# Performance work log

Measured on AMD Instinct MI355X. Metric: run time of the kernel, lower is better.

The kernel has to match this reference:

```python
import jax, jax.numpy as jnp
import numpy as np

EMBED_DIM = 1024
NUM_HEADS = 16
HEAD_DIM = EMBED_DIM // NUM_HEADS
LN_EPS = 1e-5


def setup_inputs() -> dict:
    key = jax.random.key(0)
    ks = jax.random.split(key, 6)
    b, s, d = 2, 2048, EMBED_DIM
    scale = 1.0 / np.sqrt(d)
    x = jax.random.normal(ks[0], (b, s, d), dtype=jnp.float32)
    w_qkv = jax.random.normal(ks[1], (d, 3 * d), dtype=jnp.float32) * scale
    b_qkv = jax.random.normal(ks[2], (3 * d,), dtype=jnp.float32) * 0.02
    w_out = jax.random.normal(ks[3], (d, d), dtype=jnp.float32) * scale
    b_out = jax.random.normal(ks[4], (d,), dtype=jnp.float32) * 0.02
    gamma = jnp.ones((d,), dtype=jnp.float32)
    ln_beta = jnp.zeros((d,), dtype=jnp.float32)
    beta = jax.random.normal(ks[5], (), dtype=jnp.float32) * 0.1
    return {"x": x, "w_qkv": w_qkv, "b_qkv": b_qkv, "w_out": w_out,
            "b_out": b_out, "gamma": gamma, "ln_beta": ln_beta, "beta": beta}


def _layernorm(x, gamma, ln_beta):
    mu = jnp.mean(x, axis=-1, keepdims=True)
    var = jnp.mean(jnp.square(x - mu), axis=-1, keepdims=True)
    return (x - mu) * jax.lax.rsqrt(var + LN_EPS) * gamma + ln_beta


def reference(x, w_qkv, b_qkv, w_out, b_out, gamma, ln_beta, beta):
    b, s, d = x.shape
    h, hd = NUM_HEADS, HEAD_DIM
    residual = x
    xn = _layernorm(x, gamma, ln_beta)
    qkv = xn @ w_qkv + b_qkv                       # [b, s, 3d]
    qkv = qkv.reshape(b, s, 3, h, hd)
    q = jnp.transpose(qkv[:, :, 0], (0, 2, 1, 3))  # [b, h, s, hd]
    k = jnp.transpose(qkv[:, :, 1], (0, 2, 1, 3))
    v = jnp.transpose(qkv[:, :, 2], (0, 2, 1, 3))
    attn = jnp.einsum('bhqd,bhkd->bhqk', q, k) / np.sqrt(hd)
    idx = jnp.arange(s)
    dist = jnp.abs(idx[None, :] - idx[:, None]).astype(attn.dtype)  # [s, s]
    attn = attn + beta * jnp.log1p(dist)[None, None, :, :]
    probs = jax.nn.softmax(attn, axis=-1)
    ctx = jnp.einsum('bhqk,bhkd->bhqd', probs, v)  # [b, h, s, hd]
    ctx = jnp.transpose(ctx, (0, 2, 1, 3)).reshape(b, s, d)
    return residual + ctx @ w_out + b_out
```

## Files before the change

### kernel.cpp

```cpp
#include <hip/hip_runtime.h>

#define SEQ 2048
#define DIM 1024
#define NHEAD 16
#define HDIM 64
#define NTOK 4096
#define N3D 3072

typedef __attribute__((ext_vector_type(8))) short bf16x8;
typedef __attribute__((ext_vector_type(4))) float floatx4;
typedef __attribute__((ext_vector_type(4))) unsigned short ushortx4;

__device__ __forceinline__ unsigned short f2bf(float f) {
    unsigned int u = __builtin_bit_cast(unsigned int, f);
    u += 0x7FFFu + ((u >> 16) & 1u);
    return (unsigned short)(u >> 16);
}

__device__ __forceinline__ void async_copy16(const void* g, const void* l) {
    __builtin_amdgcn_global_load_lds(
        (const __attribute__((address_space(1))) unsigned int*)(unsigned long long)g,
        (__attribute__((address_space(3))) unsigned int*)(unsigned int)(unsigned long long)l,
        16, 0, 0);
}

#define MFMA_BF16(a, b, c) __builtin_amdgcn_mfma_f32_16x16x32_bf16((a), (b), (c), 0, 0, 0)

__global__ __launch_bounds__(256)
void transpose_cvt(const float* __restrict__ src, unsigned short* __restrict__ dst,
                   int rows, int cols) {
    __shared__ float tile[32][33];
    const int c0 = blockIdx.x * 32, r0 = blockIdx.y * 32;
    const int tx = threadIdx.x & 31, ty = threadIdx.x >> 5;
    for (int i = 0; i < 4; ++i) {
        int r = ty + i * 8;
        tile[r][tx] = src[(size_t)(r0 + r) * cols + c0 + tx];
    }
    __syncthreads();
    for (int i = 0; i < 4; ++i) {
        int rr = ty + i * 8;
        dst[(size_t)(c0 + rr) * rows + r0 + tx] = f2bf(tile[tx][rr]);
    }
}

__global__ __launch_bounds__(256)
void ln_kernel(const float* __restrict__ x, const float* __restrict__ gamma,
               const float* __restrict__ lnb, unsigned short* __restrict__ xn) {
    const int row = blockIdx.x;
    const int tid = threadIdx.x;
    const float* xr = x + (size_t)row * DIM;
    float4 v = ((const float4*)xr)[tid];
    float s = v.x + v.y + v.z + v.w;
    float s2 = v.x * v.x + v.y * v.y + v.z * v.z + v.w * v.w;
    for (int off = 1; off < 64; off <<= 1) {
        s += __shfl_xor(s, off, 64);
        s2 += __shfl_xor(s2, off, 64);
    }
    __shared__ float red[8];
    const int wave = tid >> 6, lane = tid & 63;
    if (lane == 0) { red[wave] = s; red[4 + wave] = s2; }
    __syncthreads();
    s = red[0] + red[1] + red[2] + red[3];
    s2 = red[4] + red[5] + red[6] + red[7];
    const float mu = s * (1.0f / DIM);
    const float var = s2 * (1.0f / DIM) - mu * mu;
    const float rstd = rsqrtf(var + 1e-5f);
    float4 g = ((const float4*)gamma)[tid];
    float4 bb = ((const float4*)lnb)[tid];
    unsigned short* o = xn + (size_t)row * DIM + tid * 4;
    o[0] = f2bf((v.x - mu) * rstd * g.x + bb.x);
    o[1] = f2bf((v.y - mu) * rstd * g.y + bb.y);
    o[2] = f2bf((v.z - mu) * rstd * g.z + bb.z);
    o[3] = f2bf((v.w - mu) * rstd * g.w + bb.w);
}

__global__ __launch_bounds__(256)
void qkv_gemm(const unsigned short* __restrict__ A, const unsigned short* __restrict__ Bt,
              const float* __restrict__ bias, unsigned short* __restrict__ qo,
              unsigned short* __restrict__ ko, unsigned short* __restrict__ vTo) {
    __shared__ unsigned short Asm[128 * 32];
    __shared__ unsigned short Bsm[128 * 32];
    const int tid = threadIdx.x;
    const int wave = tid >> 6, lane = tid & 63;
    const int quad = lane >> 4, r16 = lane & 15;
    const int m0 = blockIdx.y * 128, n0 = blockIdx.x * 128;
    const int wm = (wave & 1) * 64, wn = (wave >> 1) * 64;
    floatx4 acc[4][4] = {};
    for (int k0 = 0; k0 < DIM; k0 += 32) {
        __syncthreads();
        for (int p = 0; p < 2; ++p) {
            int s = tid + p * 256;
            int r = s >> 2, c8 = (s & 3) << 3;
            async_copy16(A + (size_t)(m0 + r) * DIM + k0 + c8, Asm + s * 8);
            async_copy16(Bt + (size_t)(n0 + r) * DIM + k0 + c8, Bsm + s * 8);
        }
        __syncthreads();
        bf16x8 af[4], bfr[4];
        for (int i = 0; i < 4; ++i)
            af[i] = *(const bf16x8*)(Asm + (wm + i * 16 + r16) * 32 + quad * 8);
        for (int j = 0; j < 4; ++j)
            bfr[j] = *(const bf16x8*)(Bsm + (wn + j * 16 + r16) * 32 + quad * 8);
        for (int i = 0; i < 4; ++i)
            for (int j = 0; j < 4; ++j)
                acc[i][j] = MFMA_BF16(af[i], bfr[j], acc[i][j]);
    }
    for (int j = 0; j < 4; ++j) {
        int n = n0 + wn + j * 16 + r16;
        float bn = bias[n];
        int part = n >> 10, nn = n & 1023;
        int head = nn >> 6, hdi = nn & 63;
        for (int i = 0; i < 4; ++i) {
            int mbase = m0 + wm + i * 16 + quad * 4;
            int bIdx = mbase >> 11, sIdx = mbase & 2047;
            if (part == 2) {
                ushortx4 pack;
                for (int e = 0; e < 4; ++e) pack[e] = f2bf(acc[i][j][e] + bn);
                *(ushortx4*)(vTo + ((size_t)(bIdx * NHEAD + head) * HDIM + hdi) * SEQ + sIdx) = pack;
            } else {
                unsigned short* dst = (part == 0) ? qo : ko;
                for (int e = 0; e < 4; ++e)
                    dst[((size_t)(bIdx * NHEAD + head) * SEQ + sIdx + e) * HDIM + hdi] =
                        f2bf(acc[i][j][e] + bn);
            }
        }
    }
}

__global__ __launch_bounds__(512)
void attn_kernel(const unsigned short* __restrict__ qg, const unsigned short* __restrict__ kg,
                 const unsigned short* __restrict__ vTg, const float* __restrict__ betap,
                 unsigned short* __restrict__ ctx) {
    __shared__ unsigned short QP[128][72];
    __shared__ unsigned short Kd[2][64 * 64];
    __shared__ unsigned short Vd[2][64 * 64];
    __shared__ float logt[SEQ];

    const int tid = threadIdx.x;
    const int wave = tid >> 6, lane = tid & 63;
    const int quad = lane >> 4, r16 = lane & 15;
    const int bh = blockIdx.y, qt = blockIdx.x;
    const int qBase = qt * 128;
    const float betaV = betap[0];
    const float L2E = 1.44269504f;
    const float c1 = 0.125f * L2E;

    for (int i = tid; i < SEQ; i += 512)
        logt[i] = betaV * log1pf((float)i) * L2E - 20.0f;

    const unsigned short* qptr = qg + ((size_t)bh * SEQ + qBase) * HDIM;
    for (int s = tid; s < 1024; s += 512) {
        int r = s >> 3, c8 = (s & 7) << 3;
        *(bf16x8*)(&QP[r][c8]) = *(const bf16x8*)(qptr + r * HDIM + c8);
    }

    const int sr = tid >> 3;
    const int scg = (tid & 7) ^ (sr & 7);
    const unsigned short* kbh = kg + (size_t)bh * SEQ * HDIM;
    const unsigned short* vbh = vTg + (size_t)bh * HDIM * SEQ;
    async_copy16(kbh + (size_t)sr * HDIM + scg * 8, &Kd[0][tid * 8]);
    async_copy16(vbh + (size_t)sr * SEQ + scg * 8, &Vd[0][tid * 8]);
    __syncthreads();

    bf16x8 qf0 = *(const bf16x8*)(&QP[wave * 16 + r16][quad * 8]);
    bf16x8 qf1 = *(const bf16x8*)(&QP[wave * 16 + r16][32 + quad * 8]);

    const bf16x8 onesv = {0x3F80, 0x3F80, 0x3F80, 0x3F80, 0x3F80, 0x3F80, 0x3F80, 0x3F80};

    floatx4 o[5] = {};
    const int qWaveBase = qBase + wave * 16;
    const int qrow0 = qWaveBase + quad * 4;

    for (int kt0 = 0; kt0 < SEQ; kt0 += 64) {
        const int buf = (kt0 >> 6) & 1;
        if (kt0 + 64 < SEQ) {
            async_copy16(kbh + (size_t)(kt0 + 64 + sr) * HDIM + scg * 8, &Kd[buf ^ 1][tid * 8]);
            async_copy16(vbh + (size_t)sr * SEQ + kt0 + 64 + scg * 8, &Vd[buf ^ 1][tid * 8]);
        }

        floatx4 sc[4];
        for (int ct = 0; ct < 4; ++ct) {
            int rK = ct * 16 + r16;
            const unsigned short* kb = &Kd[buf][rK * 64];
            bf16x8 kf0 = *(const bf16x8*)(kb + ((quad ^ (rK & 7)) << 3));
            bf16x8 kf1 = *(const bf16x8*)(kb + (((quad ^ 4) ^ (rK & 7)) << 3));
            floatx4 z = {0.f, 0.f, 0.f, 0.f};
            z = MFMA_BF16(qf0, kf0, z);
            z = MFMA_BF16(qf1, kf1, z);
            sc[ct] = z;
        }
        for (int ct = 0; ct < 4; ++ct) {
            const int keyTile = kt0 + ct * 16;
            const int key = keyTile + r16;
            if (qWaveBase >= keyTile + 16) {
                const float* lp = &logt[qrow0 - key];
                for (int i = 0; i < 4; ++i)
                    sc[ct][i] = __builtin_amdgcn_exp2f(sc[ct][i] * c1 + lp[i]);
            } else if (keyTile >= qWaveBase + 16) {
                const float* lp = &logt[key - qrow0 - 3];
                for (int i = 0; i < 4; ++i)
                    sc[ct][i] = __builtin_amdgcn_exp2f(sc[ct][i] * c1 + lp[3 - i]);
            } else {
                for (int i = 0; i < 4; ++i) {
                    int dist = qrow0 + i - key;
                    dist = dist < 0 ? -dist : dist;
                    sc[ct][i] = __builtin_amdgcn_exp2f(sc[ct][i] * c1 + logt[dist]);
                }
            }
        }
        for (int ct = 0; ct < 4; ++ct)
            for (int i = 0; i < 4; ++i)
                QP[wave * 16 + quad * 4 + i][ct * 16 + r16] = f2bf(sc[ct][i]);
        bf16x8 pf0 = *(const bf16x8*)(&QP[wave * 16 + r16][quad * 8]);
        bf16x8 pf1 = *(const bf16x8*)(&QP[wave * 16 + r16][32 + quad * 8]);
        for (int nt = 0; nt < 4; ++nt) {
            int rV = nt * 16 + r16;
            const unsigned short* vb = &Vd[buf][rV * 64];
            bf16x8 vf0 = *(const bf16x8*)(vb + ((quad ^ (rV & 7)) << 3));
            bf16x8 vf1 = *(const bf16x8*)(vb + (((quad ^ 4) ^ (rV & 7)) << 3));
            o[nt] = MFMA_BF16(pf0, vf0, o[nt]);
            o[nt] = MFMA_BF16(pf1, vf1, o[nt]);
        }
        o[4] = MFMA_BF16(pf0, onesv, o[4]);
        o[4] = MFMA_BF16(pf1, onesv, o[4]);

        __syncthreads();
    }

    const int b_ = bh >> 4, h_ = bh & 15;
    for (int i = 0; i < 4; ++i) {
        float inv = 1.0f / o[4][i];
        int qi = qBase + wave * 16 + quad * 4 + i;
        for (int nt = 0; nt < 4; ++nt) {
            int d = nt * 16 + r16;
            ctx[((size_t)(b_ * SEQ + qi)) * DIM + h_ * HDIM + d] = f2bf(o[nt][i] * inv);
        }
    }
}

__global__ __launch_bounds__(256)
void out_gemm(const unsigned short* __restrict__ A, const unsigned short* __restrict__ Bt,
              const float* __restrict__ bias, const float* __restrict__ resid,
              float* __restrict__ out) {
    __shared__ unsigned short Asm[128 * 32];
    __shared__ unsigned short Bsm[64 * 32];
    const int tid = threadIdx.x;
    const int wave = tid >> 6, lane = tid & 63;
    const int quad = lane >> 4, r16 = lane & 15;
    const int m0 = blockIdx.y * 128, n0 = blockIdx.x * 64;
    const int wm = (wave & 1) * 64, wn = (wave >> 1) * 32;
    floatx4 acc[4][2] = {};
    for (int k0 = 0; k0 < DIM; k0 += 32) {
        __syncthreads();
        for (int p = 0; p < 2; ++p) {
            int s = tid + p * 256;
            int r = s >> 2, c8 = (s & 3) << 3;
            async_copy16(A + (size_t)(m0 + r) * DIM + k0 + c8, Asm + s * 8);
        }
        {
            int r = tid >> 2, c8 = (tid & 3) << 3;
            async_copy16(Bt + (size_t)(n0 + r) * DIM + k0 + c8, Bsm + tid * 8);
        }
        __syncthreads();
        bf16x8 af[4], bfr[2];
        for (int i = 0; i < 4; ++i)
            af[i] = *(const bf16x8*)(Asm + (wm + i * 16 + r16) * 32 + quad * 8);
        for (int j = 0; j < 2; ++j)
            bfr[j] = *(const bf16x8*)(Bsm + (wn + j * 16 + r16) * 32 + quad * 8);
        for (int i = 0; i < 4; ++i)
            for (int j = 0; j < 2; ++j)
                acc[i][j] = MFMA_BF16(af[i], bfr[j], acc[i][j]);
    }
    for (int i = 0; i < 4; ++i)
        for (int j = 0; j < 2; ++j)
            for (int e = 0; e < 4; ++e) {
                int m = m0 + wm + i * 16 + quad * 4 + e;
                int n = n0 + wn + j * 16 + r16;
                out[(size_t)m * DIM + n] = acc[i][j][e] + bias[n] + resid[(size_t)m * DIM + n];
            }
}

extern "C" void kernel_launch(void* const* d_in, const int* in_sizes, int n_in,
                              void* d_out, int out_size, void* d_ws, size_t ws_size,
                              hipStream_t stream) {
    const float* x     = (const float*)d_in[0];
    const float* w_qkv = (const float*)d_in[1];
    const float* b_qkv = (const float*)d_in[2];
    const float* w_out = (const float*)d_in[3];
    const float* b_out = (const float*)d_in[4];
    const float* gamma = (const float*)d_in[5];
    const float* ln_b  = (const float*)d_in[6];
    const float* beta  = (const float*)d_in[7];
    float* out = (float*)d_out;

    char* ws = (char*)d_ws;
    const size_t MB = 1u << 20;
    unsigned short* xn    = (unsigned short*)(ws);
    unsigned short* wqkvT = (unsigned short*)(ws + 8 * MB);
    unsigned short* woutT = (unsigned short*)(ws + 14 * MB);
    unsigned short* qb    = (unsigned short*)(ws + 16 * MB);
    unsigned short* kb    = (unsigned short*)(ws + 24 * MB);
    unsigned short* vTb   = (unsigned short*)(ws + 32 * MB);
    unsigned short* ctx   = xn;

    transpose_cvt<<<dim3(96, 32), 256, 0, stream>>>(w_qkv, wqkvT, DIM, N3D);
    transpose_cvt<<<dim3(32, 32), 256, 0, stream>>>(w_out, woutT, DIM, DIM);
    ln_kernel<<<NTOK, 256, 0, stream>>>(x, gamma, ln_b, xn);
    qkv_gemm<<<dim3(24, 32), 256, 0, stream>>>(xn, wqkvT, b_qkv, qb, kb, vTb);
    attn_kernel<<<dim3(SEQ / 128, 32), 512, 0, stream>>>(qb, kb, vTb, beta, ctx);
    out_gemm<<<dim3(16, 32), 256, 0, stream>>>(ctx, woutT, b_out, x, out);
}
```

Measured before the change: 229.8 us.

## Split attention over key halves and build P in registers via bpermute

The attention grid gains a second dimension that splits the key range in half. Each block writes unnormalized bf16 partial outputs plus row sums, and a new combine kernel adds the halves and normalizes them before the output GEMM. The QK MFMA operands are swapped so scores come out transposed, which lets the probability fragment be assembled with ds_bpermute and packed bf16 conversion instead of a round trip through the QP shared tile. That tile is removed, and launch bounds request higher occupancy. The aim is more parallelism and less LDS traffic, at the cost of an extra kernel launch and extra global traffic for the partial outputs.

```diff
diff --git a/kernel.cpp b/kernel.cpp
--- a/kernel.cpp
+++ b/kernel.cpp
@@ -10,11 +10,22 @@
 typedef __attribute__((ext_vector_type(8))) short bf16x8;
 typedef __attribute__((ext_vector_type(4))) float floatx4;
 typedef __attribute__((ext_vector_type(4))) unsigned short ushortx4;
+typedef __attribute__((ext_vector_type(4))) int intx4;
 
 __device__ __forceinline__ unsigned short f2bf(float f) {
     unsigned int u = __builtin_bit_cast(unsigned int, f);
     u += 0x7FFFu + ((u >> 16) & 1u);
     return (unsigned short)(u >> 16);
+}
+
+__device__ __forceinline__ unsigned int pack_bf16(float a, float b) {
+#if __has_builtin(__builtin_amdgcn_cvt_pk_bf16_f32)
+    typedef __attribute__((ext_vector_type(2))) __bf16 bf16x2t;
+    bf16x2t t = __builtin_amdgcn_cvt_pk_bf16_f32(a, b);
+    return __builtin_bit_cast(unsigned int, t);
+#else
+    return (unsigned int)f2bf(a) | ((unsigned int)f2bf(b) << 16);
+#endif
 }
 
 __device__ __forceinline__ void async_copy16(const void* g, const void* l) {
@@ -126,11 +137,10 @@
     }
 }
 
-__global__ __launch_bounds__(512)
+__global__ __launch_bounds__(512, 8)
 void attn_kernel(const unsigned short* __restrict__ qg, const unsigned short* __restrict__ kg,
                  const unsigned short* __restrict__ vTg, const float* __restrict__ betap,
-                 unsigned short* __restrict__ ctx) {
-    __shared__ unsigned short QP[128][72];
+                 unsigned short* __restrict__ opart, float* __restrict__ lpart) {
     __shared__ unsigned short Kd[2][64 * 64];
     __shared__ unsigned short Vd[2][64 * 64];
     __shared__ float logt[SEQ];
@@ -138,8 +148,9 @@
     const int tid = threadIdx.x;
     const int wave = tid >> 6, lane = tid & 63;
     const int quad = lane >> 4, r16 = lane & 15;
-    const int bh = blockIdx.y, qt = blockIdx.x;
+    const int bh = blockIdx.y, qt = blockIdx.x, ks = blockIdx.z;
     const int qBase = qt * 128;
+    const int kBase = ks * (SEQ / 2);
     const float betaV = betap[0];
     const float L2E = 1.44269504f;
     const float c1 = 0.125f * L2E;
@@ -147,32 +158,32 @@
     for (int i = tid; i < SEQ; i += 512)
         logt[i] = betaV * log1pf((float)i) * L2E - 20.0f;
 
-    const unsigned short* qptr = qg + ((size_t)bh * SEQ + qBase) * HDIM;
-    for (int s = tid; s < 1024; s += 512) {
-        int r = s >> 3, c8 = (s & 7) << 3;
-        *(bf16x8*)(&QP[r][c8]) = *(const bf16x8*)(qptr + r * HDIM + c8);
-    }
+    const unsigned short* qrow_p = qg + ((size_t)bh * SEQ + qBase + wave * 16 + r16) * HDIM;
+    bf16x8 qf0 = *(const bf16x8*)(qrow_p + quad * 8);
+    bf16x8 qf1 = *(const bf16x8*)(qrow_p + 32 + quad * 8);
 
     const int sr = tid >> 3;
     const int scg = (tid & 7) ^ (sr & 7);
     const unsigned short* kbh = kg + (size_t)bh * SEQ * HDIM;
     const unsigned short* vbh = vTg + (size_t)bh * HDIM * SEQ;
-    async_copy16(kbh + (size_t)sr * HDIM + scg * 8, &Kd[0][tid * 8]);
-    async_copy16(vbh + (size_t)sr * SEQ + scg * 8, &Vd[0][tid * 8]);
+    async_copy16(kbh + (size_t)(kBase + sr) * HDIM + scg * 8, &Kd[0][tid * 8]);
+    async_copy16(vbh + (size_t)sr * SEQ + kBase + scg * 8, &Vd[0][tid * 8]);
     __syncthreads();
 
-    bf16x8 qf0 = *(const bf16x8*)(&QP[wave * 16 + r16][quad * 8]);
-    bf16x8 qf1 = *(const bf16x8*)(&QP[wave * 16 + r16][32 + quad * 8]);
-
     const bf16x8 onesv = {0x3F80, 0x3F80, 0x3F80, 0x3F80, 0x3F80, 0x3F80, 0x3F80, 0x3F80};
-
-    floatx4 o[5] = {};
+    const int idx_lo = ((quad & 1) * 32 + r16) * 4;
+    const int idx_hi = ((quad & 1) * 32 + 16 + r16) * 4;
+    const bool hi_ct = quad >= 2;
+
+    floatx4 o[4] = {};
+    floatx4 o4 = {};
+    const int qrow = qBase + wave * 16 + r16;
     const int qWaveBase = qBase + wave * 16;
-    const int qrow0 = qWaveBase + quad * 4;
-
-    for (int kt0 = 0; kt0 < SEQ; kt0 += 64) {
-        const int buf = (kt0 >> 6) & 1;
-        if (kt0 + 64 < SEQ) {
+
+    for (int kt = 0; kt < SEQ / 2; kt += 64) {
+        const int kt0 = kBase + kt;
+        const int buf = (kt >> 6) & 1;
+        if (kt + 64 < SEQ / 2) {
             async_copy16(kbh + (size_t)(kt0 + 64 + sr) * HDIM + scg * 8, &Kd[buf ^ 1][tid * 8]);
             async_copy16(vbh + (size_t)sr * SEQ + kt0 + 64 + scg * 8, &Vd[buf ^ 1][tid * 8]);
         }
@@ -184,57 +195,89 @@
             bf16x8 kf0 = *(const bf16x8*)(kb + ((quad ^ (rK & 7)) << 3));
             bf16x8 kf1 = *(const bf16x8*)(kb + (((quad ^ 4) ^ (rK & 7)) << 3));
             floatx4 z = {0.f, 0.f, 0.f, 0.f};
-            z = MFMA_BF16(qf0, kf0, z);
-            z = MFMA_BF16(qf1, kf1, z);
+            z = MFMA_BF16(kf0, qf0, z);
+            z = MFMA_BF16(kf1, qf1, z);
             sc[ct] = z;
         }
         for (int ct = 0; ct < 4; ++ct) {
             const int keyTile = kt0 + ct * 16;
-            const int key = keyTile + r16;
+            const int key0 = keyTile + quad * 4;
             if (qWaveBase >= keyTile + 16) {
-                const float* lp = &logt[qrow0 - key];
+                const float* lp = &logt[qrow - key0 - 3];
+                for (int i = 0; i < 4; ++i)
+                    sc[ct][i] = __builtin_amdgcn_exp2f(sc[ct][i] * c1 + lp[3 - i]);
+            } else if (keyTile >= qWaveBase + 16) {
+                const float* lp = &logt[key0 - qrow];
                 for (int i = 0; i < 4; ++i)
                     sc[ct][i] = __builtin_amdgcn_exp2f(sc[ct][i] * c1 + lp[i]);
-            } else if (keyTile >= qWaveBase + 16) {
-                const float* lp = &logt[key - qrow0 - 3];
-                for (int i = 0; i < 4; ++i)
-                    sc[ct][i] = __builtin_amdgcn_exp2f(sc[ct][i] * c1 + lp[3 - i]);
             } else {
                 for (int i = 0; i < 4; ++i) {
-                    int dist = qrow0 + i - key;
-                    dist = dist < 0 ? -dist : dist;
-                    sc[ct][i] = __builtin_amdgcn_exp2f(sc[ct][i] * c1 + logt[dist]);
+                    int d = key0 + i - qrow;
+                    d = d < 0 ? -d : d;
+                    sc[ct][i] = __builtin_amdgcn_exp2f(sc[ct][i] * c1 + logt[d]);
                 }
             }
         }
-        for (int ct = 0; ct < 4; ++ct)
-            for (int i = 0; i < 4; ++i)
-                QP[wave * 16 + quad * 4 + i][ct * 16 + r16] = f2bf(sc[ct][i]);
-        bf16x8 pf0 = *(const bf16x8*)(&QP[wave * 16 + r16][quad * 8]);
-        bf16x8 pf1 = *(const bf16x8*)(&QP[wave * 16 + r16][32 + quad * 8]);
-        for (int nt = 0; nt < 4; ++nt) {
-            int rV = nt * 16 + r16;
-            const unsigned short* vb = &Vd[buf][rV * 64];
-            bf16x8 vf0 = *(const bf16x8*)(vb + ((quad ^ (rV & 7)) << 3));
-            bf16x8 vf1 = *(const bf16x8*)(vb + (((quad ^ 4) ^ (rV & 7)) << 3));
-            o[nt] = MFMA_BF16(pf0, vf0, o[nt]);
-            o[nt] = MFMA_BF16(pf1, vf1, o[nt]);
-        }
-        o[4] = MFMA_BF16(pf0, onesv, o[4]);
-        o[4] = MFMA_BF16(pf1, onesv, o[4]);
-
-        __syncthreads();
-    }
-
+        unsigned int pk[4][2];
+        for (int ct = 0; ct < 4; ++ct) {
+            pk[ct][0] = pack_bf16(sc[ct][0], sc[ct][1]);
+            pk[ct][1] = pack_bf16(sc[ct][2], sc[ct][3]);
+        }
+        for (int h = 0; h < 2; ++h) {
+            const int cA = 2 * h, cB = 2 * h + 1;
+            int b0a = __builtin_amdgcn_ds_bpermute(idx_lo, (int)pk[cA][0]);
+            int b0b = __builtin_amdgcn_ds_bpermute(idx_lo, (int)pk[cB][0]);
+            int b1a = __builtin_amdgcn_ds_bpermute(idx_lo, (int)pk[cA][1]);
+            int b1b = __builtin_amdgcn_ds_bpermute(idx_lo, (int)pk[cB][1]);
+            int b2a = __builtin_amdgcn_ds_bpermute(idx_hi, (int)pk[cA][0]);
+            int b2b = __builtin_amdgcn_ds_bpermute(idx_hi, (int)pk[cB][0]);
+            int b3a = __builtin_amdgcn_ds_bpermute(idx_hi, (int)pk[cA][1]);
+            int b3b = __builtin_amdgcn_ds_bpermute(idx_hi, (int)pk[cB][1]);
+            intx4 pb_i = {hi_ct ? b0b : b0a, hi_ct ? b1b : b1a,
+                          hi_ct ? b2b : b2a, hi_ct ? b3b : b3a};
+            bf16x8 pb = __builtin_bit_cast(bf16x8, pb_i);
+            for (int nt = 0; nt < 4; ++nt) {
+                int rV = nt * 16 + r16;
+                const unsigned short* vb = &Vd[buf][rV * 64];
+                bf16x8 vf = *(const bf16x8*)(vb + (((quad + 4 * h) ^ (rV & 7)) << 3));
+                o[nt] = MFMA_BF16(vf, pb, o[nt]);
+            }
+            o4 = MFMA_BF16(onesv, pb, o4);
+        }
+        __syncthreads();
+    }
+
+    unsigned short* op = opart + (size_t)ks * NTOK * DIM;
     const int b_ = bh >> 4, h_ = bh & 15;
+    const size_t rowoff = ((size_t)(b_ * SEQ + qrow)) * DIM + h_ * HDIM;
+    for (int nt = 0; nt < 4; ++nt) {
+        ushortx4 pck;
+        for (int i = 0; i < 4; ++i) pck[i] = f2bf(o[nt][i]);
+        *(ushortx4*)(op + rowoff + nt * 16 + quad * 4) = pck;
+    }
+    if (quad == 0)
+        lpart[(size_t)ks * NHEAD * 2 * SEQ + (size_t)bh * SEQ + qrow] = o4[0];
+}
+
+__global__ __launch_bounds__(256)
+void attn_combine(const unsigned short* __restrict__ oA, unsigned short* __restrict__ oB,
+                  const float* __restrict__ lA, const float* __restrict__ lB) {
+    const int row = blockIdx.x;
+    const int col = threadIdx.x * 4;
+    const int b_ = row >> 11, q = row & 2047;
+    const int head = col >> 6;
+    const int li = (b_ * NHEAD + head) * SEQ + q;
+    const float inv = 1.0f / (lA[li] + lB[li]);
+    const size_t off = (size_t)row * DIM + col;
+    ushortx4 a = *(const ushortx4*)(oA + off);
+    ushortx4 b = *(const ushortx4*)(oB + off);
+    ushortx4 r;
     for (int i = 0; i < 4; ++i) {
-        float inv = 1.0f / o[4][i];
-        int qi = qBase + wave * 16 + quad * 4 + i;
-        for (int nt = 0; nt < 4; ++nt) {
-            int d = nt * 16 + r16;
-            ctx[((size_t)(b_ * SEQ + qi)) * DIM + h_ * HDIM + d] = f2bf(o[nt][i] * inv);
-        }
-    }
+        float fa = __builtin_bit_cast(float, (unsigned int)(unsigned short)a[i] << 16);
+        float fb = __builtin_bit_cast(float, (unsigned int)(unsigned short)b[i] << 16);
+        r[i] = f2bf((fa + fb) * inv);
+    }
+    *(ushortx4*)(oB + off) = r;
 }
 
 __global__ __launch_bounds__(256)
@@ -295,17 +338,20 @@
     char* ws = (char*)d_ws;
     const size_t MB = 1u << 20;
     unsigned short* xn    = (unsigned short*)(ws);
-    unsigned short* wqkvT = (unsigned short*)(ws + 8 * MB);
-    unsigned short* woutT = (unsigned short*)(ws + 14 * MB);
-    unsigned short* qb    = (unsigned short*)(ws + 16 * MB);
-    unsigned short* kb    = (unsigned short*)(ws + 24 * MB);
-    unsigned short* vTb   = (unsigned short*)(ws + 32 * MB);
-    unsigned short* ctx   = xn;
+    unsigned short* oA    = (unsigned short*)(ws);
+    unsigned short* oB    = (unsigned short*)(ws + 8 * MB);
+    unsigned short* wqkvT = (unsigned short*)(ws + 16 * MB);
+    float*          lprt  = (float*)(ws + 16 * MB);
+    unsigned short* woutT = (unsigned short*)(ws + 22 * MB);
+    unsigned short* qb    = (unsigned short*)(ws + 24 * MB);
+    unsigned short* kb    = (unsigned short*)(ws + 32 * MB);
+    unsigned short* vTb   = (unsigned short*)(ws + 40 * MB);
 
     transpose_cvt<<<dim3(96, 32), 256, 0, stream>>>(w_qkv, wqkvT, DIM, N3D);
     transpose_cvt<<<dim3(32, 32), 256, 0, stream>>>(w_out, woutT, DIM, DIM);
     ln_kernel<<<NTOK, 256, 0, stream>>>(x, gamma, ln_b, xn);
     qkv_gemm<<<dim3(24, 32), 256, 0, stream>>>(xn, wqkvT, b_qkv, qb, kb, vTb);
-    attn_kernel<<<dim3(SEQ / 128, 32), 512, 0, stream>>>(qb, kb, vTb, beta, ctx);
-    out_gemm<<<dim3(16, 32), 256, 0, stream>>>(ctx, woutT, b_out, x, out);
-}
+    attn_kernel<<<dim3(SEQ / 128, 32, 2), 512, 0, stream>>>(qb, kb, vTb, beta, oA, lprt);
+    attn_combine<<<NTOK, 256, 0, stream>>>(oA, oB, lprt, lprt + 32 * SEQ);
+    out_gemm<<<dim3(16, 32), 256, 0, stream>>>(oB, woutT, b_out, x, out);
+}
```

New measurement: 249.8 us. +8.7%, slower.

## Compute transposed scores to keep P in registers and drop LDS round-trip

Applied to the files above, without the earlier changes.

The attention kernel now computes S^T (K as the A operand, Q as B), so each lane's softmax outputs line up with the B operand of a 16x16x16 MFMA for P·V. That removes the LDS write/read of P and the QP buffer. Each wave now handles 32 query rows with 256 threads per block, so K/V fragments loaded from LDS are reused across two query tiles. The log-bias table is stored as paired float2 entries so one read serves two lookups, and ctx stores are vectorized. The cost is more accumulator registers per wave and the use of the smaller-K MFMA variant.

```diff
diff --git a/kernel.cpp b/kernel.cpp
--- a/kernel.cpp
+++ b/kernel.cpp
@@ -8,13 +8,19 @@
 #define N3D 3072
 
 typedef __attribute__((ext_vector_type(8))) short bf16x8;
+typedef __attribute__((ext_vector_type(4))) short bf16x4;
 typedef __attribute__((ext_vector_type(4))) float floatx4;
 typedef __attribute__((ext_vector_type(4))) unsigned short ushortx4;
+typedef __attribute__((ext_vector_type(2))) int intx2;
 
 __device__ __forceinline__ unsigned short f2bf(float f) {
     unsigned int u = __builtin_bit_cast(unsigned int, f);
     u += 0x7FFFu + ((u >> 16) & 1u);
     return (unsigned short)(u >> 16);
+}
+
+__device__ __forceinline__ unsigned int pack_bf16(float a, float b) {
+    return (unsigned int)f2bf(a) | ((unsigned int)f2bf(b) << 16);
 }
 
 __device__ __forceinline__ void async_copy16(const void* g, const void* l) {
@@ -25,6 +31,7 @@
 }
 
 #define MFMA_BF16(a, b, c) __builtin_amdgcn_mfma_f32_16x16x32_bf16((a), (b), (c), 0, 0, 0)
+#define MFMA16(a, b, c) __builtin_amdgcn_mfma_f32_16x16x16bf16_1k((a), (b), (c), 0, 0, 0)
 
 __global__ __launch_bounds__(256)
 void transpose_cvt(const float* __restrict__ src, unsigned short* __restrict__ dst,
@@ -126,14 +133,13 @@
     }
 }
 
-__global__ __launch_bounds__(512)
+__global__ __launch_bounds__(256)
 void attn_kernel(const unsigned short* __restrict__ qg, const unsigned short* __restrict__ kg,
                  const unsigned short* __restrict__ vTg, const float* __restrict__ betap,
                  unsigned short* __restrict__ ctx) {
-    __shared__ unsigned short QP[128][72];
     __shared__ unsigned short Kd[2][64 * 64];
     __shared__ unsigned short Vd[2][64 * 64];
-    __shared__ float logt[SEQ];
+    __shared__ float2 L2t[SEQ];
 
     const int tid = threadIdx.x;
     const int wave = tid >> 6, lane = tid & 63;
@@ -144,13 +150,23 @@
     const float L2E = 1.44269504f;
     const float c1 = 0.125f * L2E;
 
-    for (int i = tid; i < SEQ; i += 512)
-        logt[i] = betaV * log1pf((float)i) * L2E - 20.0f;
-
-    const unsigned short* qptr = qg + ((size_t)bh * SEQ + qBase) * HDIM;
-    for (int s = tid; s < 1024; s += 512) {
-        int r = s >> 3, c8 = (s & 7) << 3;
-        *(bf16x8*)(&QP[r][c8]) = *(const bf16x8*)(qptr + r * HDIM + c8);
+    for (int t = tid; t < SEQ; t += 256) {
+        float fa = betaV * log1pf((float)t) * L2E - 20.0f;
+        int t1 = (t + 1 < SEQ) ? t + 1 : SEQ - 1;
+        float fb = betaV * log1pf((float)t1) * L2E - 20.0f;
+        L2t[t] = make_float2(fa, fb);
+    }
+    const float* Ff = (const float*)L2t;
+
+    bf16x8 qf[2][2];
+    {
+        const unsigned short* qp0 =
+            qg + ((size_t)bh * SEQ + qBase + wave * 32 + r16) * HDIM;
+        qf[0][0] = *(const bf16x8*)(qp0 + quad * 8);
+        qf[0][1] = *(const bf16x8*)(qp0 + 32 + quad * 8);
+        const unsigned short* qp1 = qp0 + 16 * HDIM;
+        qf[1][0] = *(const bf16x8*)(qp1 + quad * 8);
+        qf[1][1] = *(const bf16x8*)(qp1 + 32 + quad * 8);
     }
 
     const int sr = tid >> 3;
@@ -158,81 +174,99 @@
     const unsigned short* kbh = kg + (size_t)bh * SEQ * HDIM;
     const unsigned short* vbh = vTg + (size_t)bh * HDIM * SEQ;
     async_copy16(kbh + (size_t)sr * HDIM + scg * 8, &Kd[0][tid * 8]);
+    async_copy16(kbh + (size_t)(sr + 32) * HDIM + scg * 8, &Kd[0][2048 + tid * 8]);
     async_copy16(vbh + (size_t)sr * SEQ + scg * 8, &Vd[0][tid * 8]);
+    async_copy16(vbh + (size_t)(sr + 32) * SEQ + scg * 8, &Vd[0][2048 + tid * 8]);
     __syncthreads();
 
-    bf16x8 qf0 = *(const bf16x8*)(&QP[wave * 16 + r16][quad * 8]);
-    bf16x8 qf1 = *(const bf16x8*)(&QP[wave * 16 + r16][32 + quad * 8]);
-
-    const bf16x8 onesv = {0x3F80, 0x3F80, 0x3F80, 0x3F80, 0x3F80, 0x3F80, 0x3F80, 0x3F80};
-
-    floatx4 o[5] = {};
-    const int qWaveBase = qBase + wave * 16;
-    const int qrow0 = qWaveBase + quad * 4;
+    const bf16x4 ones4 = {0x3F80, 0x3F80, 0x3F80, 0x3F80};
+
+    floatx4 o[2][4] = {};
+    floatx4 o4[2] = {};
+    const int qWB0 = qBase + wave * 32;
+    const int qrow0 = qWB0 + r16;
 
     for (int kt0 = 0; kt0 < SEQ; kt0 += 64) {
         const int buf = (kt0 >> 6) & 1;
         if (kt0 + 64 < SEQ) {
-            async_copy16(kbh + (size_t)(kt0 + 64 + sr) * HDIM + scg * 8, &Kd[buf ^ 1][tid * 8]);
+            const unsigned short* kp = kbh + (size_t)(kt0 + 64) * HDIM;
+            async_copy16(kp + (size_t)sr * HDIM + scg * 8, &Kd[buf ^ 1][tid * 8]);
+            async_copy16(kp + (size_t)(sr + 32) * HDIM + scg * 8, &Kd[buf ^ 1][2048 + tid * 8]);
             async_copy16(vbh + (size_t)sr * SEQ + kt0 + 64 + scg * 8, &Vd[buf ^ 1][tid * 8]);
-        }
-
-        floatx4 sc[4];
+            async_copy16(vbh + (size_t)(sr + 32) * SEQ + kt0 + 64 + scg * 8,
+                         &Vd[buf ^ 1][2048 + tid * 8]);
+        }
+
+        floatx4 sc[2][4];
         for (int ct = 0; ct < 4; ++ct) {
             int rK = ct * 16 + r16;
             const unsigned short* kb = &Kd[buf][rK * 64];
             bf16x8 kf0 = *(const bf16x8*)(kb + ((quad ^ (rK & 7)) << 3));
             bf16x8 kf1 = *(const bf16x8*)(kb + (((quad ^ 4) ^ (rK & 7)) << 3));
-            floatx4 z = {0.f, 0.f, 0.f, 0.f};
-            z = MFMA_BF16(qf0, kf0, z);
-            z = MFMA_BF16(qf1, kf1, z);
-            sc[ct] = z;
-        }
-        for (int ct = 0; ct < 4; ++ct) {
-            const int keyTile = kt0 + ct * 16;
-            const int key = keyTile + r16;
-            if (qWaveBase >= keyTile + 16) {
-                const float* lp = &logt[qrow0 - key];
-                for (int i = 0; i < 4; ++i)
-                    sc[ct][i] = __builtin_amdgcn_exp2f(sc[ct][i] * c1 + lp[i]);
-            } else if (keyTile >= qWaveBase + 16) {
-                const float* lp = &logt[key - qrow0 - 3];
-                for (int i = 0; i < 4; ++i)
-                    sc[ct][i] = __builtin_amdgcn_exp2f(sc[ct][i] * c1 + lp[3 - i]);
-            } else {
-                for (int i = 0; i < 4; ++i) {
-                    int dist = qrow0 + i - key;
-                    dist = dist < 0 ? -dist : dist;
-                    sc[ct][i] = __builtin_amdgcn_exp2f(sc[ct][i] * c1 + logt[dist]);
+            for (int qn = 0; qn < 2; ++qn) {
+                floatx4 z = {0.f, 0.f, 0.f, 0.f};
+                z = MFMA_BF16(kf0, qf[qn][0], z);
+                z = MFMA_BF16(kf1, qf[qn][1], z);
+                sc[qn][ct] = z;
+            }
+        }
+        bf16x4 pk[2][4];
+        for (int qn = 0; qn < 2; ++qn) {
+            const int qWB = qWB0 + qn * 16;
+            const int qrow = qrow0 + qn * 16;
+            for (int ct = 0; ct < 4; ++ct) {
+                const int keyTile = kt0 + ct * 16;
+                const int key0 = keyTile + quad * 4;
+                floatx4 s = sc[qn][ct];
+                if (qWB >= keyTile + 16) {
+                    int dlo = qrow - key0 - 3;
+                    float2 a = L2t[dlo], b = L2t[dlo + 2];
+                    s[0] = __builtin_amdgcn_exp2f(s[0] * c1 + b.y);
+                    s[1] = __builtin_amdgcn_exp2f(s[1] * c1 + b.x);
+                    s[2] = __builtin_amdgcn_exp2f(s[2] * c1 + a.y);
+                    s[3] = __builtin_amdgcn_exp2f(s[3] * c1 + a.x);
+                } else if (keyTile >= qWB + 16) {
+                    int dlo = key0 - qrow;
+                    float2 a = L2t[dlo], b = L2t[dlo + 2];
+                    s[0] = __builtin_amdgcn_exp2f(s[0] * c1 + a.x);
+                    s[1] = __builtin_amdgcn_exp2f(s[1] * c1 + a.y);
+                    s[2] = __builtin_amdgcn_exp2f(s[2] * c1 + b.x);
+                    s[3] = __builtin_amdgcn_exp2f(s[3] * c1 + b.y);
+                } else {
+                    for (int i = 0; i < 4; ++i) {
+                        int d = key0 + i - qrow;
+                        d = d < 0 ? -d : d;
+                        s[i] = __builtin_amdgcn_exp2f(s[i] * c1 + Ff[2 * d]);
+                    }
                 }
-            }
-        }
-        for (int ct = 0; ct < 4; ++ct)
-            for (int i = 0; i < 4; ++i)
-                QP[wave * 16 + quad * 4 + i][ct * 16 + r16] = f2bf(sc[ct][i]);
-        bf16x8 pf0 = *(const bf16x8*)(&QP[wave * 16 + r16][quad * 8]);
-        bf16x8 pf1 = *(const bf16x8*)(&QP[wave * 16 + r16][32 + quad * 8]);
+                intx2 u = {(int)pack_bf16(s[0], s[1]), (int)pack_bf16(s[2], s[3])};
+                pk[qn][ct] = __builtin_bit_cast(bf16x4, u);
+            }
+        }
+        for (int ks = 0; ks < 4; ++ks) {
+            o4[0] = MFMA16(ones4, pk[0][ks], o4[0]);
+            o4[1] = MFMA16(ones4, pk[1][ks], o4[1]);
+            for (int nt = 0; nt < 4; ++nt) {
+                int rV = nt * 16 + r16;
+                const unsigned short* vb = &Vd[buf][rV * 64];
+                bf16x4 vf = *(const bf16x4*)(vb +
+                    (((ks * 2 + (quad >> 1)) ^ (rV & 7)) << 3) + ((quad & 1) << 2));
+                o[0][nt] = MFMA16(vf, pk[0][ks], o[0][nt]);
+                o[1][nt] = MFMA16(vf, pk[1][ks], o[1][nt]);
+            }
+        }
+        __syncthreads();
+    }
+
+    const int b_ = bh >> 4, h_ = bh & 15;
+    for (int qn = 0; qn < 2; ++qn) {
+        float inv = 1.0f / o4[qn][0];
+        int q = qBase + wave * 32 + qn * 16 + r16;
+        size_t base = ((size_t)(b_ * SEQ + q)) * DIM + h_ * HDIM;
         for (int nt = 0; nt < 4; ++nt) {
-            int rV = nt * 16 + r16;
-            const unsigned short* vb = &Vd[buf][rV * 64];
-            bf16x8 vf0 = *(const bf16x8*)(vb + ((quad ^ (rV & 7)) << 3));
-            bf16x8 vf1 = *(const bf16x8*)(vb + (((quad ^ 4) ^ (rV & 7)) << 3));
-            o[nt] = MFMA_BF16(pf0, vf0, o[nt]);
-            o[nt] = MFMA_BF16(pf1, vf1, o[nt]);
-        }
-        o[4] = MFMA_BF16(pf0, onesv, o[4]);
-        o[4] = MFMA_BF16(pf1, onesv, o[4]);
-
-        __syncthreads();
-    }
-
-    const int b_ = bh >> 4, h_ = bh & 15;
-    for (int i = 0; i < 4; ++i) {
-        float inv = 1.0f / o[4][i];
-        int qi = qBase + wave * 16 + quad * 4 + i;
-        for (int nt = 0; nt < 4; ++nt) {
-            int d = nt * 16 + r16;
-            ctx[((size_t)(b_ * SEQ + qi)) * DIM + h_ * HDIM + d] = f2bf(o[nt][i] * inv);
+            ushortx4 pck;
+            for (int i = 0; i < 4; ++i) pck[i] = f2bf(o[qn][nt][i] * inv);
+            *(ushortx4*)(ctx + base + nt * 16 + quad * 4) = pck;
         }
     }
 }
@@ -306,6 +340,6 @@
     transpose_cvt<<<dim3(32, 32), 256, 0, stream>>>(w_out, woutT, DIM, DIM);
     ln_kernel<<<NTOK, 256, 0, stream>>>(x, gamma, ln_b, xn);
     qkv_gemm<<<dim3(24, 32), 256, 0, stream>>>(xn, wqkvT, b_qkv, qb, kb, vTb);
-    attn_kernel<<<dim3(SEQ / 128, 32), 512, 0, stream>>>(qb, kb, vTb, beta, ctx);
+    attn_kernel<<<dim3(SEQ / 128, 32), 256, 0, stream>>>(qb, kb, vTb, beta, ctx);
     out_gemm<<<dim3(16, 32), 256, 0, stream>>>(ctx, woutT, b_out, x, out);
 }
```

Result: slower. 247.5 us (+7.7%).
